# Optimization experiments

Measured on AMD Instinct MI355X. Metric: run time of the kernel, lower is better.

The kernel has to match this reference:

```python
import jax, jax.numpy as jnp
import numpy as np
import math

B, N, D, H = 2, 2048, 1024, 16
HD = D // H          # head dim = 64
ROT = 32             # rotary dim (applied to first ROT channels of each head)


def rotate_half(x):
    # '... (d r) -> ... d r' with r=2: even/odd interleaved pairs
    x1 = x[..., 0::2]
    x2 = x[..., 1::2]
    return jnp.stack((-x2, x1), axis=-1).reshape(x.shape)


def apply_rotary_pos_emb(t, freqs):
    rot_dim, seq_len = freqs.shape[-1], t.shape[-2]
    freqs = freqs[-seq_len:, :]
    t_rot, t_pass = t[..., :rot_dim], t[..., rot_dim:]
    t_rot = t_rot * jnp.cos(freqs) + rotate_half(t_rot) * jnp.sin(freqs)
    return jnp.concatenate((t_rot, t_pass), axis=-1)


def setup_inputs() -> dict:
    key = jax.random.key(0)
    ks = jax.random.split(key, 8)
    return {
        "q": jax.random.normal(ks[0], (B, N, D), jnp.float32),
        "k": jax.random.normal(ks[1], (B, N, D), jnp.float32),
        "v": jax.random.normal(ks[2], (B, N, D), jnp.float32),
        "wq": jax.random.normal(ks[3], (D, D), jnp.float32) * (1.0 / math.sqrt(D)),
        "wk": jax.random.normal(ks[4], (D, D), jnp.float32) * (1.0 / math.sqrt(D)),
        "wv": jax.random.normal(ks[5], (D, D), jnp.float32) * (1.0 / math.sqrt(D)),
        "wo": jax.random.normal(ks[6], (D, D), jnp.float32) * (1.0 / math.sqrt(D)),
        "rot_pos_emb": jax.random.normal(ks[7], (N, ROT), jnp.float32),
    }


def reference(q, k, v, wq, wk, wv, wo, rot_pos_emb):
    # projections (nn.Linear with bias=False: x @ W.T)
    qh = (q @ wq.T).reshape(B, N, H, HD).transpose(0, 2, 1, 3)  # b h n d
    kh = (k @ wk.T).reshape(B, N, H, HD).transpose(0, 2, 1, 3)
    vh = (v @ wv.T).reshape(B, N, H, HD).transpose(0, 2, 1, 3)
    qh = apply_rotary_pos_emb(qh, rot_pos_emb)
    kh = apply_rotary_pos_emb(kh, rot_pos_emb)
    k_t = kh.transpose(0, 1, 3, 2)                               # b h d n
    scores = (qh @ k_t) / math.sqrt(HD)                          # b h n n
    attn = jax.nn.softmax(scores, axis=-1)
    out = attn @ vh                                              # b h n d
    out = out.transpose(0, 2, 1, 3).reshape(B, N, H * HD)        # b n (h d)
    return (out @ wo.T, k_t, vh)
```

## Files before the change

kernel.cpp:

```cpp
#include <hip/hip_runtime.h>
#include <math.h>

#define NN 2048
#define DD 1024
#define HH 16
#define OUTSZ (2*NN*DD)

typedef unsigned short u16;
typedef unsigned int u32;
typedef __attribute__((ext_vector_type(8))) short short8;
typedef __attribute__((ext_vector_type(4))) float floatx4;
typedef __attribute__((ext_vector_type(4))) unsigned short us4;

__device__ __forceinline__ u16 f2bf(float x) {
    union { float f; unsigned u; } v; v.f = x;
    unsigned r = v.u + 0x7FFFu + ((v.u >> 16) & 1u);
    return (u16)(r >> 16);
}

__device__ __forceinline__ u32 fbits(float x) {
    union { float f; u32 u; } v; v.f = x; return v.u;
}

__device__ __forceinline__ u32 pack_bf2(float lo, float hi) {
    return __builtin_amdgcn_perm(fbits(hi) + 0x8000u, fbits(lo) + 0x8000u, 0x07060302u);
}

__device__ __forceinline__ float fexp2(float x) {
#if __has_builtin(__builtin_amdgcn_exp2f)
    return __builtin_amdgcn_exp2f(x);
#else
    return __expf(x * 0.69314718056f);
#endif
}

__device__ __forceinline__ void gl_lds16(const u16* g, u16* l) {
    __builtin_amdgcn_global_load_lds(
        (const __attribute__((address_space(1))) unsigned int*)g,
        (__attribute__((address_space(3))) unsigned int*)l, 16, 0, 0);
}

struct CastArgs { const float* s[7]; u16* d[7]; int n[7]; };

__global__ __launch_bounds__(256)
void cast_bf16(CastArgs a) {
    const int ten = blockIdx.y;
    const float4* s = (const float4*)a.s[ten];
    us4* d = (us4*)a.d[ten];
    const int n4 = a.n[ten] >> 2;
    for (int i = blockIdx.x * 256 + threadIdx.x; i < n4; i += gridDim.x * 256) {
        float4 f = s[i];
        us4 u = {f2bf(f.x), f2bf(f.y), f2bf(f.z), f2bf(f.w)};
        d[i] = u;
    }
}

struct ProjArgs {
    const u16* X[4]; const u16* W[4];
    float* outf[4];  u16* outb[4];
    const float* rot;
};

template<int TN>
__global__ __launch_bounds__(256)
void mfma_proj(ProjArgs a, int mode_base)
{
    constexpr int TNW = TN / 2;
    constexpr int NJ  = TNW / 16;

    __shared__ __align__(16) u16 As[128 * 64];
    __shared__ __align__(16) u16 Bs[TN * 64];

    const int mode = mode_base + blockIdx.z;
    const u16* __restrict__ X   = a.X[mode];
    const u16* __restrict__ Wm  = a.W[mode];
    float* __restrict__ outf    = a.outf[mode];
    u16* __restrict__ outb      = a.outb[mode];
    const float* __restrict__ rot = a.rot;

    const int t    = threadIdx.x;
    const int lane = t & 63;
    const int w    = t >> 6;
    const int wr   = (w >> 1) * 64;
    const int wc   = (w & 1) * TNW;
    const int m0   = blockIdx.y * 128;
    const int j0   = blockIdx.x * TN;

    const int lc = (t & 7) ^ ((t >> 3) & 7);
    const u16* gA = X  + (size_t)(m0 + (t >> 3)) * DD + lc * 8;
    const u16* gB = Wm + (size_t)(j0 + (t >> 3)) * DD + lc * 8;

    const int fr = lane & 15;
    const int fq = lane >> 4;

    floatx4 acc[4][NJ] = {};

    for (int k0 = 0; k0 < DD; k0 += 64) {
        __syncthreads();
        #pragma unroll
        for (int p = 0; p < 4; ++p)
            gl_lds16(gA + (size_t)(32 * p) * DD + k0, As + (p * 256 + t) * 8);
        #pragma unroll
        for (int p = 0; p < TN / 32; ++p)
            gl_lds16(gB + (size_t)(32 * p) * DD + k0, Bs + (p * 256 + t) * 8);
        __syncthreads();
        #pragma unroll
        for (int kk = 0; kk < 2; ++kk) {
            const int ph = (kk * 4 + fq) ^ (fr & 7);
            short8 af[4], bf[NJ];
            #pragma unroll
            for (int i = 0; i < 4; ++i)
                af[i] = *(const short8*)(As + (wr + i * 16 + fr) * 64 + ph * 8);
            #pragma unroll
            for (int j = 0; j < NJ; ++j)
                bf[j] = *(const short8*)(Bs + (wc + j * 16 + fr) * 64 + ph * 8);
            #pragma unroll
            for (int i = 0; i < 4; ++i)
                #pragma unroll
                for (int j = 0; j < NJ; ++j)
                    acc[i][j] = __builtin_amdgcn_mfma_f32_16x16x32_bf16(af[i], bf[j], acc[i][j], 0, 0, 0);
        }
    }

    const int b = m0 >> 11;
    #pragma unroll
    for (int i = 0; i < 4; ++i) {
        const int mrow  = m0 + wr + i * 16 + fq * 4;
        const int nbase = mrow & (NN - 1);
        #pragma unroll
        for (int j = 0; j < NJ; ++j) {
            const int col = j0 + wc + j * 16 + fr;
            const int h = col >> 6, d = col & 63;
            const int bh = b * HH + h;
            float v[4];
            #pragma unroll
            for (int r = 0; r < 4; ++r) v[r] = acc[i][j][r];
            if (mode <= 1 && ((wc + j * 16) & 63) < 32) {
                #pragma unroll
                for (int r = 0; r < 4; ++r) {
                    const int n = nbase + r;
                    float c = v[r];
                    float p = __shfl_xor(c, 1);
                    float f = rot[n * 32 + d];
                    float sn, cs; __sincosf(f, &sn, &cs);
                    v[r] = (d & 1) ? fmaf(c, cs, p * sn) : fmaf(c, cs, -p * sn);
                }
            }
            if (mode == 0) {
                #pragma unroll
                for (int r = 0; r < 4; ++r)
                    outb[((size_t)bh * NN + nbase + r) * 64 + d] = f2bf(v[r] * 0.1803368801111244f);
            } else if (mode == 1) {
                float4 f4 = {v[0], v[1], v[2], v[3]};
                *(float4*)&outf[((size_t)bh * 64 + d) * NN + nbase] = f4;
                #pragma unroll
                for (int r = 0; r < 4; ++r)
                    outb[((size_t)bh * NN + nbase + r) * 64 + d] = f2bf(v[r]);
            } else if (mode == 2) {
                #pragma unroll
                for (int r = 0; r < 4; ++r)
                    outf[((size_t)bh * NN + nbase + r) * 64 + d] = v[r];
                us4 u = {f2bf(v[0]), f2bf(v[1]), f2bf(v[2]), f2bf(v[3])};
                *(us4*)&outb[((size_t)bh * 64 + d) * NN + nbase] = u;
            } else {
                #pragma unroll
                for (int r = 0; r < 4; ++r)
                    outf[(size_t)(mrow + r) * DD + col] = v[r];
            }
        }
    }
}

__global__ __launch_bounds__(256, 3)
void mfma_attn(const u16* __restrict__ qh, const u16* __restrict__ kh,
               const u16* __restrict__ vt, u16* __restrict__ ctx)
{
    __shared__ __align__(16) u16 Ks[128 * 64];
    __shared__ __align__(16) u16 Vs[64 * 128];
    __shared__ __align__(16) u16 Ps[4 * 64 * 40];
    __shared__ float Lsc[64];

    const int t    = threadIdx.x;
    const int lane = t & 63;
    const int w    = t >> 6;
    const int fr   = lane & 15;
    const int fq   = lane >> 4;
    const int bh   = blockIdx.x;
    const int q0   = blockIdx.y * 64;
    const int b    = bh >> 4, h = bh & 15;

    short8 qf[4][2];
    #pragma unroll
    for (int c = 0; c < 4; ++c)
        #pragma unroll
        for (int kk = 0; kk < 2; ++kk)
            qf[c][kk] = *(const short8*)(qh +
                ((size_t)bh * NN + q0 + c * 16 + fr) * 64 + kk * 32 + fq * 8);

    const int lc8  = (t & 7) ^ ((t >> 3) & 7);
    const int lc16 = (t & 15) ^ ((t >> 4) & 15);
    const u16* kg = kh + ((size_t)bh * NN + (t >> 3)) * 64 + lc8 * 8;
    const u16* vg = vt + ((size_t)bh * 64 + (t >> 4)) * NN + lc16 * 8;

    u16* Pw = Ps + w * 64 * 40;

    floatx4 o4[4][4] = {};
    float lrun[4] = {0.f, 0.f, 0.f, 0.f};

    for (int j0k = 0; j0k < NN; j0k += 128) {
        __syncthreads();
        #pragma unroll
        for (int p = 0; p < 4; ++p)
            gl_lds16(kg + (size_t)(j0k + p * 32) * 64, Ks + (p * 256 + t) * 8);
        #pragma unroll
        for (int p = 0; p < 4; ++p)
            gl_lds16(vg + (size_t)(p * 16) * NN + j0k, Vs + (p * 256 + t) * 8);
        __syncthreads();

        short8 kf[2][2];
        #pragma unroll
        for (int jt = 0; jt < 2; ++jt)
            #pragma unroll
            for (int kk = 0; kk < 2; ++kk) {
                const int row = w * 32 + jt * 16 + fr;
                const int phys = (kk * 4 + fq) ^ (row & 7);
                kf[jt][kk] = *(const short8*)(Ks + row * 64 + phys * 8);
            }
        floatx4 sT[2][4] = {};
        #pragma unroll
        for (int jt = 0; jt < 2; ++jt)
            #pragma unroll
            for (int c = 0; c < 4; ++c)
                #pragma unroll
                for (int kk = 0; kk < 2; ++kk)
                    sT[jt][c] = __builtin_amdgcn_mfma_f32_16x16x32_bf16(kf[jt][kk], qf[c][kk], sT[jt][c], 0, 0, 0);

        #pragma unroll
        for (int c = 0; c < 4; ++c) {
            u16* pb = Pw + (c * 16 + fr) * 40;
            #pragma unroll
            for (int jt = 0; jt < 2; ++jt) {
                float p0 = fexp2(sT[jt][c][0]);
                float p1 = fexp2(sT[jt][c][1]);
                float p2 = fexp2(sT[jt][c][2]);
                float p3 = fexp2(sT[jt][c][3]);
                lrun[c] += (p0 + p1) + (p2 + p3);
                uint2 pv = {pack_bf2(p0, p1), pack_bf2(p2, p3)};
                *(uint2*)(pb + jt * 16 + fq * 4) = pv;
            }
        }

        short8 pa[4], vf[4];
        #pragma unroll
        for (int m = 0; m < 4; ++m)
            pa[m] = *(const short8*)(Pw + (m * 16 + fr) * 40 + fq * 8);
        #pragma unroll
        for (int n = 0; n < 4; ++n) {
            const int row = n * 16 + fr;
            const int phys = (w * 4 + fq) ^ (row & 15);
            vf[n] = *(const short8*)(Vs + row * 128 + phys * 8);
        }
        #pragma unroll
        for (int m = 0; m < 4; ++m)
            #pragma unroll
            for (int n = 0; n < 4; ++n)
                o4[m][n] = __builtin_amdgcn_mfma_f32_16x16x32_bf16(pa[m], vf[n], o4[m][n], 0, 0, 0);
    }

    #pragma unroll
    for (int c = 0; c < 4; ++c) {
        lrun[c] += __shfl_xor(lrun[c], 16);
        lrun[c] += __shfl_xor(lrun[c], 32);
    }

    float* Osc = (float*)Ps;
    __syncthreads();
    for (int ww = 0; ww < 4; ++ww) {
        if (w == ww) {
            #pragma unroll
            for (int m = 0; m < 4; ++m)
                #pragma unroll
                for (int n = 0; n < 4; ++n)
                    #pragma unroll
                    for (int r = 0; r < 4; ++r) {
                        const int q = m * 16 + fq * 4 + r;
                        const int d = n * 16 + fr;
                        if (ww == 0) Osc[q * 64 + d] = o4[m][n][r];
                        else         Osc[q * 64 + d] += o4[m][n][r];
                    }
            if (fq == 0) {
                #pragma unroll
                for (int c = 0; c < 4; ++c) {
                    const int q = c * 16 + fr;
                    if (ww == 0) Lsc[q] = lrun[c];
                    else         Lsc[q] += lrun[c];
                }
            }
        }
        __syncthreads();
    }

    const int q  = t >> 2;
    const float inv = 1.0f / Lsc[q];
    #pragma unroll
    for (int i = 0; i < 4; ++i) {
        const int d0 = (t & 3) * 16 + i * 4;
        float4 o = *(const float4*)(Osc + q * 64 + d0);
        us4 u = {f2bf(o.x * inv), f2bf(o.y * inv), f2bf(o.z * inv), f2bf(o.w * inv)};
        *(us4*)&ctx[((size_t)b * NN + q0 + q) * DD + h * 64 + d0] = u;
    }
}

extern "C" void kernel_launch(void* const* d_in, const int* in_sizes, int n_in,
                              void* d_out, int out_size, void* d_ws, size_t ws_size,
                              hipStream_t stream)
{
    const float* q   = (const float*)d_in[0];
    const float* k   = (const float*)d_in[1];
    const float* v   = (const float*)d_in[2];
    const float* wq  = (const float*)d_in[3];
    const float* wk  = (const float*)d_in[4];
    const float* wv  = (const float*)d_in[5];
    const float* wo  = (const float*)d_in[6];
    const float* rot = (const float*)d_in[7];

    float* out_final = (float*)d_out;
    float* out_kt    = out_final + OUTSZ;
    float* out_vh    = out_kt + OUTSZ;

    u16* wsb  = (u16*)d_ws;
    u16* qb   = wsb;
    u16* kb   = wsb + (size_t) 4 * 1024 * 1024;
    u16* vb   = wsb + (size_t) 8 * 1024 * 1024;
    u16* wqb  = wsb + (size_t)12 * 1024 * 1024;
    u16* wkb  = wsb + (size_t)13 * 1024 * 1024;
    u16* wvb  = wsb + (size_t)14 * 1024 * 1024;
    u16* wob  = wsb + (size_t)15 * 1024 * 1024;
    u16* qhb  = wsb + (size_t)16 * 1024 * 1024;
    u16* khb  = wsb + (size_t)20 * 1024 * 1024;
    u16* vtb  = wsb + (size_t)24 * 1024 * 1024;
    u16* ctxb = wsb + (size_t)28 * 1024 * 1024;

    CastArgs ca;
    ca.s[0] = q;  ca.d[0] = qb;  ca.n[0] = OUTSZ;
    ca.s[1] = k;  ca.d[1] = kb;  ca.n[1] = OUTSZ;
    ca.s[2] = v;  ca.d[2] = vb;  ca.n[2] = OUTSZ;
    ca.s[3] = wq; ca.d[3] = wqb; ca.n[3] = DD * DD;
    ca.s[4] = wk; ca.d[4] = wkb; ca.n[4] = DD * DD;
    ca.s[5] = wv; ca.d[5] = wvb; ca.n[5] = DD * DD;
    ca.s[6] = wo; ca.d[6] = wob; ca.n[6] = DD * DD;
    cast_bf16<<<dim3(256, 7), 256, 0, stream>>>(ca);

    ProjArgs pa;
    pa.X[0] = qb;   pa.W[0] = wqb; pa.outf[0] = nullptr;   pa.outb[0] = qhb;
    pa.X[1] = kb;   pa.W[1] = wkb; pa.outf[1] = out_kt;    pa.outb[1] = khb;
    pa.X[2] = vb;   pa.W[2] = wvb; pa.outf[2] = out_vh;    pa.outb[2] = vtb;
    pa.X[3] = ctxb; pa.W[3] = wob; pa.outf[3] = out_final; pa.outb[3] = nullptr;
    pa.rot = rot;

    mfma_proj<128><<<dim3(DD / 128, (2 * NN) / 128, 3), 256, 0, stream>>>(pa, 0);

    mfma_attn<<<dim3(2 * HH, NN / 64), 256, 0, stream>>>(qhb, khb, vtb, ctxb);

    mfma_proj<64><<<dim3(DD / 64, (2 * NN) / 128, 1), 256, 0, stream>>>(pa, 3);
}
```

Before: 242.3 us.

## Load K/V fragments directly from global into registers with prefetch, drop LDS staging

```diff
diff --git a/kernel.cpp b/kernel.cpp
--- a/kernel.cpp
+++ b/kernel.cpp
@@ -175,8 +175,6 @@
 void mfma_attn(const u16* __restrict__ qh, const u16* __restrict__ kh,
                const u16* __restrict__ vt, u16* __restrict__ ctx)
 {
-    __shared__ __align__(16) u16 Ks[128 * 64];
-    __shared__ __align__(16) u16 Vs[64 * 128];
     __shared__ __align__(16) u16 Ps[4 * 64 * 40];
     __shared__ float Lsc[64];
 
@@ -197,35 +195,25 @@
             qf[c][kk] = *(const short8*)(qh +
                 ((size_t)bh * NN + q0 + c * 16 + fr) * 64 + kk * 32 + fq * 8);
 
-    const int lc8  = (t & 7) ^ ((t >> 3) & 7);
-    const int lc16 = (t & 15) ^ ((t >> 4) & 15);
-    const u16* kg = kh + ((size_t)bh * NN + (t >> 3)) * 64 + lc8 * 8;
-    const u16* vg = vt + ((size_t)bh * 64 + (t >> 4)) * NN + lc16 * 8;
+    const u16* kA = kh + ((size_t)bh * NN + w * 32 + fr) * 64 + fq * 8;
+    const u16* vB = vt + ((size_t)bh * 64 + fr) * NN + w * 32 + fq * 8;
 
     u16* Pw = Ps + w * 64 * 40;
 
     floatx4 o4[4][4] = {};
     float lrun[4] = {0.f, 0.f, 0.f, 0.f};
 
+    short8 kf[2][2], vf[4];
+    #pragma unroll
+    for (int jt = 0; jt < 2; ++jt)
+        #pragma unroll
+        for (int kk = 0; kk < 2; ++kk)
+            kf[jt][kk] = *(const short8*)(kA + (size_t)(jt * 16) * 64 + kk * 32);
+    #pragma unroll
+    for (int n = 0; n < 4; ++n)
+        vf[n] = *(const short8*)(vB + (size_t)(n * 16) * NN);
+
     for (int j0k = 0; j0k < NN; j0k += 128) {
-        __syncthreads();
-        #pragma unroll
-        for (int p = 0; p < 4; ++p)
-            gl_lds16(kg + (size_t)(j0k + p * 32) * 64, Ks + (p * 256 + t) * 8);
-        #pragma unroll
-        for (int p = 0; p < 4; ++p)
-            gl_lds16(vg + (size_t)(p * 16) * NN + j0k, Vs + (p * 256 + t) * 8);
-        __syncthreads();
-
-        short8 kf[2][2];
-        #pragma unroll
-        for (int jt = 0; jt < 2; ++jt)
-            #pragma unroll
-            for (int kk = 0; kk < 2; ++kk) {
-                const int row = w * 32 + jt * 16 + fr;
-                const int phys = (kk * 4 + fq) ^ (row & 7);
-                kf[jt][kk] = *(const short8*)(Ks + row * 64 + phys * 8);
-            }
         floatx4 sT[2][4] = {};
         #pragma unroll
         for (int jt = 0; jt < 2; ++jt)
@@ -234,6 +222,15 @@
                 #pragma unroll
                 for (int kk = 0; kk < 2; ++kk)
                     sT[jt][c] = __builtin_amdgcn_mfma_f32_16x16x32_bf16(kf[jt][kk], qf[c][kk], sT[jt][c], 0, 0, 0);
+
+        const int nxt = j0k + 128;
+        if (nxt < NN) {
+            #pragma unroll
+            for (int jt = 0; jt < 2; ++jt)
+                #pragma unroll
+                for (int kk = 0; kk < 2; ++kk)
+                    kf[jt][kk] = *(const short8*)(kA + (size_t)(nxt + jt * 16) * 64 + kk * 32);
+        }
 
         #pragma unroll
         for (int c = 0; c < 4; ++c) {
@@ -250,21 +247,21 @@
             }
         }
 
-        short8 pa[4], vf[4];
+        short8 pa[4];
         #pragma unroll
         for (int m = 0; m < 4; ++m)
             pa[m] = *(const short8*)(Pw + (m * 16 + fr) * 40 + fq * 8);
         #pragma unroll
-        for (int n = 0; n < 4; ++n) {
-            const int row = n * 16 + fr;
-            const int phys = (w * 4 + fq) ^ (row & 15);
-            vf[n] = *(const short8*)(Vs + row * 128 + phys * 8);
-        }
-        #pragma unroll
         for (int m = 0; m < 4; ++m)
             #pragma unroll
             for (int n = 0; n < 4; ++n)
                 o4[m][n] = __builtin_amdgcn_mfma_f32_16x16x32_bf16(pa[m], vf[n], o4[m][n], 0, 0, 0);
+
+        if (nxt < NN) {
+            #pragma unroll
+            for (int n = 0; n < 4; ++n)
+                vf[n] = *(const short8*)(vB + (size_t)(n * 16) * NN + nxt);
+        }
     }
 
     #pragma unroll
```

Measured after the change: 285.8 us. 17.9% more time.
